# Kernel tuning notes

Hardware: AMD Instinct MI355X
Metric: run time of the kernel (lower is better)

Reference implementation:

```python
import jax, jax.numpy as jnp
import numpy as np

H = 14
N = H * H
DIM = 768
INT = 5
LAM = 3.5


def fft_conv_grouped(x, w):
    # x: (B, g*in_c, N) real; w: (g, int_c, in_c, H, H//2+1) complex
    g, int_c, in_c = w.shape[:3]
    B = x.shape[0]
    xf = jnp.fft.rfftn(x.reshape(B, g, in_c, H, H), axes=(-2, -1), norm='ortho')
    yf = jnp.einsum('bgchf,gichf->bgihf', xf, w)
    y = jnp.fft.irfftn(yf, s=(H, H), axes=(-2, -1), norm='ortho')
    return y.reshape(B, g * int_c, N)


def soft(x, t):
    # sign(x) * relu(|x| - t)
    return jnp.sign(x) * jnp.maximum(jnp.abs(x) - t, 0.0)


def batch_norm(x, gamma, beta, eps=1e-5):
    # training-mode BatchNorm1d applied per channel over (B, N); x: (B, N, C)
    m = x.mean(axis=(0, 1))
    v = x.var(axis=(0, 1))
    return (x - m) * jax.lax.rsqrt(v + eps) * gamma + beta


def setup_inputs() -> dict:
    key = jax.random.key(0)
    ks = jax.random.split(key, 8)
    B = 32
    Hf = H // 2 + 1
    # kernel: init randn*0.06, then normalize_parameters()
    kr = jax.random.normal(ks[0], (DIM, INT, 1, H, Hf, 2), dtype=jnp.float32) * 0.06
    kc = kr[..., 0] + 1j * kr[..., 1]
    nrm = jnp.sqrt((jnp.abs(kc) ** 2).sum(axis=(2, 3, 4), keepdims=True) * 2.0 / H ** 2)
    kc = kc / nrm
    kernel = jnp.stack([jnp.real(kc), jnp.imag(kc)], axis=-1)
    # L buffer: update_L(lam=1) -> per-group max singular value of Gram kk
    kk = jnp.einsum('gichf,gjchf->gijhf', kc, jnp.conj(kc))
    sv = np.linalg.svd(np.asarray(jnp.transpose(kk, (0, 3, 4, 1, 2))), compute_uv=False)
    L = jnp.asarray(sv.reshape(DIM, -1).max(axis=-1), dtype=jnp.float32)
    hid = 4 * DIM
    return {
        'x': jax.random.normal(ks[1], (B, N, DIM), dtype=jnp.float32),
        'v_w': jax.random.normal(ks[2], (DIM, DIM), dtype=jnp.float32) * 0.02,
        'proj_w': jax.random.normal(ks[3], (DIM, DIM), dtype=jnp.float32) * 0.02,
        'proj_b': jnp.zeros((DIM,), dtype=jnp.float32),
        'kernel': kernel,
        'kernel2': jax.random.normal(ks[4], (DIM, 1, 1, H, Hf, 2), dtype=jnp.float32) * 0.02,
        'n1_g': jnp.ones((DIM,), dtype=jnp.float32),
        'n1_b': jnp.zeros((DIM,), dtype=jnp.float32),
        'n2_g': jnp.ones((DIM,), dtype=jnp.float32),
        'n2_b': jnp.zeros((DIM,), dtype=jnp.float32),
        'fc1_w': jax.random.normal(ks[5], (hid, DIM), dtype=jnp.float32) * 0.02,
        'fc1_b': jnp.zeros((hid,), dtype=jnp.float32),
        'fc2_w': jax.random.normal(ks[6], (DIM, hid), dtype=jnp.float32) * 0.02,
        'fc2_b': jnp.zeros((DIM,), dtype=jnp.float32),
        'L': L,
    }


def reference(x, v_w, proj_w, proj_b, kernel, kernel2, n1_g, n1_b, n2_g, n2_b, fc1_w, fc1_b, fc2_w, fc2_b, L):
    k = kernel[..., 0] + 1j * kernel[..., 1]                 # (g, int, 1, H, Hf)
    kk = jnp.einsum('gichf,gjchf->gijhf', k, jnp.conj(k))     # (g, int, int, H, Hf)
    vx = x @ v_w.T                                            # v Linear, no bias
    xc = jnp.swapaxes(vx, -2, -1)                             # (B, C, N)
    u = fft_conv_grouped(xc, k)                               # (B, g*int, N)
    Lv = jnp.repeat(L, INT)[None, :, None]                    # (1, g*int, 1)
    # ISTA: init soft-threshold then 3 gradient + shrink steps
    s = soft(u, LAM)
    for _ in range(3):
        s = s - (fft_conv_grouped(s, kk) - u) / Lv
        s = soft(s, LAM / Lv)
    # reconstruct with conjugate-transposed kernel, then mix with kernel2
    new = fft_conv_grouped(s, jnp.swapaxes(jnp.conj(k), 1, 2))  # (B, g, N)
    k2 = kernel2[..., 0] + 1j * kernel2[..., 1]
    new = fft_conv_grouped(new, k2)
    new = jnp.swapaxes(new, -2, -1)                           # (B, N, C)
    new = x + (batch_norm(new, n1_g, n1_b) @ proj_w.T + proj_b)
    h = jax.nn.gelu(batch_norm(new, n2_g, n2_b) @ fc1_w.T + fc1_b, approximate=False)
    return new + (h @ fc2_w.T + fc2_b)
```

## Files before the change

kernel.cpp:

```cpp
#include <hip/hip_runtime.h>
#include <cmath>

typedef unsigned short u16;
typedef __bf16 bf16x8 __attribute__((ext_vector_type(8)));
typedef float f32x4 __attribute__((ext_vector_type(4)));
typedef float float4v __attribute__((ext_vector_type(4)));
typedef u16 ushort4v __attribute__((ext_vector_type(4)));
typedef u16 ushort8v __attribute__((ext_vector_type(8)));

#define DIMC 768
#define NP 196
#define MTOT 6272
#define HIDC 3072
#define LAMC 3.5f

__device__ const float C14d[14] = {
  1.0f, 0.9009688679024191f, 0.6234898018587336f, 0.22252093395631445f,
  -0.22252093395631445f, -0.6234898018587336f, -0.9009688679024191f, -1.0f,
  -0.9009688679024191f, -0.6234898018587336f, -0.22252093395631445f,
  0.22252093395631445f, 0.6234898018587336f, 0.9009688679024191f
};
__device__ const float S14d[14] = {
  0.0f, 0.43388373911755823f, 0.7818314824680298f, 0.9749279121818236f,
  0.9749279121818236f, 0.7818314824680298f, 0.43388373911755823f, 0.0f,
  -0.43388373911755823f, -0.7818314824680298f, -0.9749279121818236f,
  -0.9749279121818236f, -0.7818314824680298f, -0.43388373911755823f
};

__device__ __forceinline__ u16 f2bf(float f) {
  unsigned u = __builtin_bit_cast(unsigned, f);
  unsigned r = u + 0x7FFFu + ((u >> 16) & 1u);
  return (u16)(r >> 16);
}

__device__ __forceinline__ size_t fidx(int m, int k, int K) {
  return ((size_t)(m >> 4) * (K >> 5) + (k >> 5)) * 512 +
         (size_t)((((k >> 3) & 3) * 16 + (m & 15)) * 8 + (k & 7));
}

__global__ __launch_bounds__(256) void prep_k(
    const float* __restrict__ v_w, const float* __restrict__ fc2w,
    const float* __restrict__ x,
    u16* __restrict__ vwf, u16* __restrict__ fc2f, u16* __restrict__ xf,
    u16* __restrict__ Ff, u16* __restrict__ Gf) {
  const int bid = blockIdx.x, t = threadIdx.x;
  if (bid < 378) {
    int idx = bid * 256 + t;
    if (idx < 50176) {
      int j = idx & 7, lane = (idx >> 3) & 63;
      int mk = idx >> 9, k0 = mk % 7, m0 = mk / 7;
      int s = m0 * 16 + (lane & 15);
      int q = k0 * 32 + (lane >> 4) * 8 + j;
      float v = 0.f;
      if (q < 196) {
        int kr = s >> 4, f = (s >> 1) & 7, r = q / 14, c = q % 14;
        int th = (kr * r + f * c) % 14;
        v = (s & 1) ? -S14d[th] : C14d[th];
      }
      Ff[idx] = f2bf(v);
    } else {
      int t2 = idx - 50176;
      int j = t2 & 7, lane = (t2 >> 3) & 63;
      int pk = t2 >> 9, k0 = pk % 7, p0 = pk / 7;
      int p = p0 * 16 + (lane & 15);
      int s = k0 * 32 + (lane >> 4) * 8 + j;
      float v = 0.f;
      if (p < 196) {
        int kr = s >> 4, f = (s >> 1) & 7, r = p / 14, c = p % 14;
        int th = (kr * r + f * c) % 14;
        float w = (f == 0 || f == 7) ? 1.f : 2.f;
        v = (w * (1.f / 196.f)) * ((s & 1) ? -S14d[th] : C14d[th]);
      }
      Gf[t2] = f2bf(v);
    }
    return;
  }
  const float* src; u16* dst; int idx, K;
  if (bid < 666)        { src = v_w;  dst = vwf;  idx = (bid - 378) * 256 + t;  K = DIMC; }
  else if (bid < 1818)  { src = fc2w; dst = fc2f; idx = (bid - 666) * 256 + t;  K = HIDC; }
  else                  { src = x;    dst = xf;   idx = (bid - 1818) * 256 + t; K = DIMC; }
  const int KC = K >> 5;
  int chunk = idx >> 6, l = idx & 63;
  int row = (chunk / KC) * 16 + (l & 15);
  int k0 = (chunk % KC) * 32 + (l >> 4) * 8;
  const float* sp = src + (size_t)row * K + k0;
  float4v f0 = *(const float4v*)sp;
  float4v f1 = *(const float4v*)(sp + 4);
  ushort8v o;
#pragma unroll
  for (int j = 0; j < 4; ++j) { o[j] = f2bf(f0[j]); o[j + 4] = f2bf(f1[j]); }
  *(ushort8v*)(dst + (size_t)idx * 8) = o;
}

template<int EPI>
__global__ __launch_bounds__(256, 3) void gemmw_k(
    const u16* __restrict__ Af, const u16* __restrict__ Bf,
    const float* __restrict__ bias, const float* __restrict__ res,
    void* __restrict__ Cp, int Nr, int Kr, int NB) {
  const int t = threadIdx.x, w = t >> 6, lane = t & 63;
  const int bid = blockIdx.x;
  const int xcd = bid & 7, j = bid >> 3;
  const int mt = xcd + 8 * (j / NB);
  if (mt >= 98) return;
  const int m0 = mt * 64;
  const int n0 = ((j % NB) * 4 + w) * 64;
  const int KC = Kr >> 5;
  const int l15 = lane & 15, l4 = lane >> 4;

  const u16* Ab = Af + ((size_t)(m0 >> 4) * KC) * 512 + lane * 8;
  const u16* Bb = Bf + ((size_t)(n0 >> 4) * KC) * 512 + lane * 8;

  f32x4 acc[4][4];
#pragma unroll
  for (int a = 0; a < 4; ++a)
#pragma unroll
    for (int b2 = 0; b2 < 4; ++b2) acc[a][b2] = (f32x4){0.f, 0.f, 0.f, 0.f};

  bf16x8 a0[4], b0[4], a1[4], b1[4];
#pragma unroll
  for (int mb = 0; mb < 4; ++mb) a0[mb] = *(const bf16x8*)(Ab + ((size_t)mb * KC) * 512);
#pragma unroll
  for (int nb = 0; nb < 4; ++nb) b0[nb] = *(const bf16x8*)(Bb + ((size_t)nb * KC) * 512);

  for (int kc = 0; kc < KC; kc += 2) {
#pragma unroll
    for (int mb = 0; mb < 4; ++mb)
      a1[mb] = *(const bf16x8*)(Ab + ((size_t)mb * KC + kc + 1) * 512);
#pragma unroll
    for (int nb = 0; nb < 4; ++nb)
      b1[nb] = *(const bf16x8*)(Bb + ((size_t)nb * KC + kc + 1) * 512);
    __builtin_amdgcn_s_setprio(1);
#pragma unroll
    for (int mb = 0; mb < 4; ++mb)
#pragma unroll
      for (int nb = 0; nb < 4; ++nb)
        acc[mb][nb] = __builtin_amdgcn_mfma_f32_16x16x32_bf16(a0[mb], b0[nb], acc[mb][nb], 0, 0, 0);
    __builtin_amdgcn_s_setprio(0);
    if (kc + 2 < KC) {
#pragma unroll
      for (int mb = 0; mb < 4; ++mb)
        a0[mb] = *(const bf16x8*)(Ab + ((size_t)mb * KC + kc + 2) * 512);
#pragma unroll
      for (int nb = 0; nb < 4; ++nb)
        b0[nb] = *(const bf16x8*)(Bb + ((size_t)nb * KC + kc + 2) * 512);
    }
    __builtin_amdgcn_s_setprio(1);
#pragma unroll
    for (int mb = 0; mb < 4; ++mb)
#pragma unroll
      for (int nb = 0; nb < 4; ++nb)
        acc[mb][nb] = __builtin_amdgcn_mfma_f32_16x16x32_bf16(a1[mb], b1[nb], acc[mb][nb], 0, 0, 0);
    __builtin_amdgcn_s_setprio(0);
  }

#pragma unroll
  for (int mb = 0; mb < 4; ++mb) {
#pragma unroll
    for (int nb = 0; nb < 4; ++nb) {
      int n = n0 + nb * 16 + l15;
      if (EPI == 0) {
        int m0r = m0 + mb * 16 + l4 * 4;
        int bb = m0r / 196, np0 = m0r - bb * 196;
        *(float4v*)&((float*)Cp)[((size_t)bb * DIMC + n) * 196 + np0] =
            (float4v){acc[mb][nb][0], acc[mb][nb][1], acc[mb][nb][2], acc[mb][nb][3]};
      } else {
#pragma unroll
        for (int r = 0; r < 4; ++r) {
          int m = m0 + mb * 16 + l4 * 4 + r;
          float v = acc[mb][nb][r];
          if (EPI == 1) {
            ((float*)Cp)[(size_t)m * Nr + n] = v + bias[n] + res[(size_t)m * Nr + n];
          } else {
            float vb = v + bias[n];
            float ge = 0.5f * vb * (1.f + erff(vb * 0.70710678118654752f));
            ((u16*)Cp)[fidx(m, n, Nr)] = f2bf(ge);
          }
        }
      }
    }
  }
}

__global__ __launch_bounds__(64) void xf_k(
    const float* __restrict__ vxt, const u16* __restrict__ Ff,
    float* __restrict__ xfg) {
  const int lane = threadIdx.x;
  const int wgb = blockIdx.x;
  const int g = wgb >> 1, bhalf = wgb & 1;
  const int tl = lane & 15, h = lane >> 4;
  const float* xbase = vxt + ((size_t)(bhalf * 16 + tl) * DIMC + g) * 196;

  bf16x8 Bx[7];
#pragma unroll
  for (int k0 = 0; k0 < 7; ++k0) {
    int q0 = k0 * 32 + h * 8;
    ushort8v tv;
    if (k0 < 6) {
      float4v f0 = *(const float4v*)(xbase + q0);
      float4v f1 = *(const float4v*)(xbase + q0 + 4);
#pragma unroll
      for (int j = 0; j < 4; ++j) { tv[j] = f2bf(f0[j]); tv[j + 4] = f2bf(f1[j]); }
    } else {
#pragma unroll
      for (int j = 0; j < 8; ++j) {
        int q = q0 + j;
        tv[j] = (q < 196) ? f2bf(xbase[q]) : (u16)0;
      }
    }
    Bx[k0] = __builtin_bit_cast(bf16x8, tv);
  }

  float* xo = xfg + (size_t)wgb * (16 * 224);
  for (int m0 = 0; m0 < 14; ++m0) {
    f32x4 acc = (f32x4){0.f, 0.f, 0.f, 0.f};
#pragma unroll
    for (int k0 = 0; k0 < 7; ++k0) {
      bf16x8 Af = __builtin_bit_cast(bf16x8,
          *(const ushort8v*)(Ff + ((size_t)(m0 * 7 + k0) * 64 + lane) * 8));
      acc = __builtin_amdgcn_mfma_f32_16x16x32_bf16(Af, Bx[k0], acc, 0, 0, 0);
    }
    *(f32x4*)&xo[tl * 224 + m0 * 16 + h * 4] = acc;
  }
}

__global__ __launch_bounds__(64) void screen_k(
    const float* __restrict__ xfg, const float* __restrict__ kern,
    const u16* __restrict__ Gf, int* __restrict__ cnt, int* __restrict__ wl) {
  const int lane = threadIdx.x;
  const int bid = blockIdx.x;
  const int gb = bid / 5, i = bid - gb * 5;
  const int g = gb >> 1, bhalf = gb & 1;
  const int tl = lane & 15, h = lane >> 4;
  const float* xo = xfg + (size_t)gb * (16 * 224);
  const float* kb = kern + ((size_t)g * 5 + i) * 224;

  bf16x8 By[7];
#pragma unroll
  for (int k0 = 0; k0 < 7; ++k0) {
    f32x4 x0 = *(const f32x4*)&xo[tl * 224 + k0 * 32 + h * 8];
    f32x4 x1 = *(const f32x4*)&xo[tl * 224 + k0 * 32 + h * 8 + 4];
    int mb = k0 * 16 + h * 4;
    float2 ka = *(const float2*)(kb + (mb + 0) * 2);
    float2 kc = *(const float2*)(kb + (mb + 1) * 2);
    float2 ke = *(const float2*)(kb + (mb + 2) * 2);
    float2 kg = *(const float2*)(kb + (mb + 3) * 2);
    ushort8v tv;
    tv[0] = f2bf(ka.x * x0[0] - ka.y * x0[1]);
    tv[1] = f2bf(ka.x * x0[1] + ka.y * x0[0]);
    tv[2] = f2bf(kc.x * x0[2] - kc.y * x0[3]);
    tv[3] = f2bf(kc.x * x0[3] + kc.y * x0[2]);
    tv[4] = f2bf(ke.x * x1[0] - ke.y * x1[1]);
    tv[5] = f2bf(ke.x * x1[1] + ke.y * x1[0]);
    tv[6] = f2bf(kg.x * x1[2] - kg.y * x1[3]);
    tv[7] = f2bf(kg.x * x1[3] + kg.y * x1[2]);
    By[k0] = __builtin_bit_cast(bf16x8, tv);
  }

  float vmax = 0.f;
  for (int pp = 0; pp < 6; ++pp) {
    int p0 = pp * 2;
    f32x4 a0 = (f32x4){0.f, 0.f, 0.f, 0.f};
    f32x4 a1 = a0;
#pragma unroll
    for (int k0 = 0; k0 < 7; ++k0) {
      bf16x8 Ag0 = __builtin_bit_cast(bf16x8,
          *(const ushort8v*)(Gf + ((size_t)(p0 * 7 + k0) * 64 + lane) * 8));
      bf16x8 Ag1 = __builtin_bit_cast(bf16x8,
          *(const ushort8v*)(Gf + ((size_t)((p0 + 1) * 7 + k0) * 64 + lane) * 8));
      a0 = __builtin_amdgcn_mfma_f32_16x16x32_bf16(Ag0, By[k0], a0, 0, 0, 0);
      a1 = __builtin_amdgcn_mfma_f32_16x16x32_bf16(Ag1, By[k0], a1, 0, 0, 0);
    }
#pragma unroll
    for (int r = 0; r < 4; ++r) {
      vmax = fmaxf(vmax, fabsf(a0[r]));
      vmax = fmaxf(vmax, fabsf(a1[r]));
    }
  }
  {
    f32x4 a0 = (f32x4){0.f, 0.f, 0.f, 0.f};
#pragma unroll
    for (int k0 = 0; k0 < 7; ++k0) {
      bf16x8 Ag = __builtin_bit_cast(bf16x8,
          *(const ushort8v*)(Gf + ((size_t)(12 * 7 + k0) * 64 + lane) * 8));
      a0 = __builtin_amdgcn_mfma_f32_16x16x32_bf16(Ag, By[k0], a0, 0, 0, 0);
    }
#pragma unroll
    for (int r = 0; r < 4; ++r) vmax = fmaxf(vmax, fabsf(a0[r]));
  }

  vmax = fmaxf(vmax, __shfl_xor(vmax, 16));
  vmax = fmaxf(vmax, __shfl_xor(vmax, 32));
  if (lane < 16 && vmax > (LAMC - 0.1f)) {
    int idx = atomicAdd(cnt, 1);
    wl[idx] = g * 32 + bhalf * 16 + lane;
  }
}

__global__ __launch_bounds__(64) void slow_k(
    const float* __restrict__ vxt, const float* __restrict__ kern,
    const float* __restrict__ kern2, const float* __restrict__ Lbuf,
    const int* __restrict__ cnt, const int* __restrict__ wl,
    float* __restrict__ outp,
    float* __restrict__ tsum, float* __restrict__ tsq,
    unsigned* __restrict__ maskg, unsigned* __restrict__ bmask) {
  const int ntile = *cnt;
  if ((int)blockIdx.x >= ntile) return;
  const int t = threadIdx.x;
  __shared__ float TC[196], TSn[196];
  __shared__ float xs[196];
  __shared__ float t1R[112], t1I[112];
  __shared__ float t2R[112], t2I[112];
  __shared__ float zr[112], zi[112];
  __shared__ float kR[5][112], kI[5][112];
  __shared__ float uu[5][196];
  __shared__ float ss[5][196];
  __shared__ float k2R[112], k2I[112];

  for (int i = t; i < 196; i += 64) {
    int a = i / 14, c = i - (i / 14) * 14;
    int m = (a * c) % 14;
    TC[i] = C14d[m]; TSn[i] = S14d[m];
  }

  auto rowsFwd = [&](const float* xsrc) {
    for (int i = t; i < 112; i += 64) {
      int r = i >> 3, f = i & 7;
      const float* xp = xsrc + r * 14;
      const float* tc = &TC[f * 14]; const float* tsn = &TSn[f * 14];
      float ar = 0.f, ai = 0.f;
#pragma unroll
      for (int c = 0; c < 14; ++c) { float xv = xp[c]; ar += xv * tc[c]; ai -= xv * tsn[c]; }
      t1R[i] = ar; t1I[i] = ai;
    }
    __syncthreads();
  };
  auto colsFwd = [&](float* oR, float* oI) {
    for (int i = t; i < 112; i += 64) {
      int kr = i >> 3, f = i & 7;
      const float* tc = &TC[kr * 14]; const float* tsn = &TSn[kr * 14];
      float br = 0.f, bi = 0.f;
#pragma unroll
      for (int r = 0; r < 14; ++r) {
        float xr = t1R[r * 8 + f], xi = t1I[r * 8 + f];
        br += tc[r] * xr + tsn[r] * xi;
        bi += tc[r] * xi - tsn[r] * xr;
      }
      oR[i] = br; oI[i] = bi;
    }
    __syncthreads();
  };
  auto colsInv = [&]() {
    for (int i = t; i < 112; i += 64) {
      int r = i >> 3, f = i & 7;
      const float* tc = &TC[r * 14]; const float* tsn = &TSn[r * 14];
      float br = 0.f, bi = 0.f;
#pragma unroll
      for (int kr = 0; kr < 14; ++kr) {
        float xr = t1R[kr * 8 + f], xi = t1I[kr * 8 + f];
        br += tc[kr] * xr - tsn[kr] * xi;
        bi += tc[kr] * xi + tsn[kr] * xr;
      }
      t2R[i] = br; t2I[i] = bi;
    }
    __syncthreads();
  };
  auto rowVal = [&](int r, int c) -> float {
    const float* pR = &t2R[r * 8]; const float* pI = &t2I[r * 8];
    float v = pR[0] + ((c & 1) ? -pR[7] : pR[7]);
    float s2 = 0.f;
#pragma unroll
    for (int f = 1; f < 7; ++f) s2 += pR[f] * TC[f * 14 + c] - pI[f] * TSn[f * 14 + c];
    return (v + 2.f * s2) * (1.0f / 196.0f);
  };

  for (int widx = blockIdx.x; widx < ntile; widx += gridDim.x) {
    const int tile = wl[widx];
    const int g = tile >> 5, b = tile & 31;
    __syncthreads();
    for (int i = t; i < 560; i += 64) {
      int ii = i / 112, p = i - ii * 112;
      const float* kp = kern + ((size_t)g * 5 + ii) * 224 + p * 2;
      kR[ii][p] = kp[0]; kI[ii][p] = kp[1];
    }
    for (int i = t; i < 196; i += 64) xs[i] = vxt[((size_t)b * DIMC + g) * 196 + i];
    for (int i = t; i < 112; i += 64) {
      k2R[i] = kern2[(size_t)g * 224 + i * 2];
      k2I[i] = kern2[(size_t)g * 224 + i * 2 + 1];
    }
    __syncthreads();

    rowsFwd(xs);
    colsFwd(zr, zi);
    for (int ii = 0; ii < 5; ++ii) {
      for (int i = t; i < 112; i += 64) {
        float a = kR[ii][i], b2 = kI[ii][i];
        t1R[i] = a * zr[i] - b2 * zi[i];
        t1I[i] = a * zi[i] + b2 * zr[i];
      }
      __syncthreads();
      colsInv();
      for (int i = t; i < 196; i += 64) uu[ii][i] = rowVal(i / 14, i - (i / 14) * 14);
      __syncthreads();
    }

    const float invL = 1.0f / Lbuf[g];
    const float thr = LAMC * invL;
    {
      float* up = &uu[0][0];
      float* sp = &ss[0][0];
      for (int i = t; i < 980; i += 64) {
        float v = up[i];
        float a = fabsf(v) - LAMC;
        sp[i] = a > 0.f ? copysignf(a, v) : 0.f;
      }
    }
    __syncthreads();

    for (int iter = 0; iter < 4; ++iter) {
      for (int i = t; i < 112; i += 64) { zr[i] = 0.f; zi[i] = 0.f; }
      __syncthreads();
      for (int ii = 0; ii < 5; ++ii) {
        rowsFwd(&ss[ii][0]);
        colsFwd(t2R, t2I);
        for (int i = t; i < 112; i += 64) {
          float a = kR[ii][i], b2 = kI[ii][i];
          zr[i] += a * t2R[i] + b2 * t2I[i];
          zi[i] += a * t2I[i] - b2 * t2R[i];
        }
        __syncthreads();
      }
      if (iter == 3) break;
      for (int ii = 0; ii < 5; ++ii) {
        for (int i = t; i < 112; i += 64) {
          float a = kR[ii][i], b2 = kI[ii][i];
          t1R[i] = a * zr[i] - b2 * zi[i];
          t1I[i] = a * zi[i] + b2 * zr[i];
        }
        __syncthreads();
        colsInv();
        for (int i = t; i < 196; i += 64) {
          float v = rowVal(i / 14, i - (i / 14) * 14);
          float sv = ss[ii][i] - (v - uu[ii][i]) * invL;
          float aa = fabsf(sv) - thr;
          ss[ii][i] = aa > 0.f ? copysignf(aa, sv) : 0.f;
        }
        __syncthreads();
      }
    }

    if (t < 28) {
      int kr = t >> 1, f = (t & 1) * 7;
      int d = kr * 8 + f;
      int srci = ((14 - kr) % 14) * 8 + f;
      float pr = 0.5f * (zr[d] + zr[srci]);
      float pi = 0.5f * (zi[d] - zi[srci]);
      zr[d] = pr; zi[d] = pi;
    }
    __syncthreads();
    for (int i = t; i < 112; i += 64) {
      float a = k2R[i], b2 = k2I[i];
      t1R[i] = a * zr[i] - b2 * zi[i];
      t1I[i] = a * zi[i] + b2 * zr[i];
    }
    __syncthreads();
    colsInv();
    float sacc = 0.f, qacc = 0.f;
    for (int i = t; i < 196; i += 64) {
      float v = rowVal(i / 14, i - (i / 14) * 14);
      outp[((size_t)(b * 196 + i)) * DIMC + g] = v;
      sacc += v; qacc += v * v;
    }
#pragma unroll
    for (int off = 32; off; off >>= 1) {
      sacc += __shfl_xor(sacc, off);
      qacc += __shfl_xor(qacc, off);
    }
    if (t == 0) {
      tsum[tile] = sacc; tsq[tile] = qacc;
      atomicOr(&maskg[g], 1u << b);
      atomicOr(bmask, 1u << b);
    }
  }
}

__global__ __launch_bounds__(256) void stats1c0_k(
    const float* __restrict__ tsum, const float* __restrict__ tsq,
    const unsigned* __restrict__ maskg,
    const float* __restrict__ gam, const float* __restrict__ bet,
    const float* __restrict__ projw, const float* __restrict__ pb,
    float* __restrict__ sc1, float* __restrict__ c0) {
  __shared__ float sh1s[768];
  const int t = threadIdx.x;
  for (int c = t; c < DIMC; c += 256) {
    unsigned mask = maskg[c];
    float S = 0.f, Q = 0.f;
    if (mask) {
      for (int b = 0; b < 32; ++b)
        if ((mask >> b) & 1) { S += tsum[c * 32 + b]; Q += tsq[c * 32 + b]; }
    }
    float m = S * (1.0f / 6272.0f);
    float v = fmaxf(Q * (1.0f / 6272.0f) - m * m, 0.f);
    float rs = rsqrtf(v + 1e-5f);
    float sc = gam[c] * rs;
    sh1s[c] = bet[c] - m * sc;
    if (blockIdx.x == 0) sc1[c] = sc;
  }
  __syncthreads();
  int n = blockIdx.x * 256 + t;
  const float* row = projw + (size_t)n * DIMC;
  float s = 0.f;
  for (int g = 0; g < DIMC; g += 4) {
    float4v r = *(const float4v*)(row + g);
    s += r[0] * sh1s[g] + r[1] * sh1s[g + 1] + r[2] * sh1s[g + 2] + r[3] * sh1s[g + 3];
  }
  c0[n] = s + pb[n];
}

__global__ __launch_bounds__(256) void bnb_k(
    const float* __restrict__ x, const float* __restrict__ c0,
    const float* __restrict__ sc1, const unsigned* __restrict__ maskg,
    const unsigned* __restrict__ bmask, const float* __restrict__ newm,
    const float* __restrict__ projw,
    float* __restrict__ new2, u16* __restrict__ n2f,
    float* __restrict__ part) {
  const int jb = blockIdx.x, b = blockIdx.y, t = threadIdx.x;
  __shared__ unsigned gm[24];
  __shared__ float c0s[768];
  const bool hasb = ((*bmask >> b) & 1u) != 0u;
  if (t < 24) {
    unsigned w = 0;
    if (hasb)
      for (int j2 = 0; j2 < 32; ++j2) w |= ((maskg[t * 32 + j2] >> b) & 1u) << j2;
    gm[t] = w;
  }
  for (int c = t; c < 768; c += 256) c0s[c] = c0[c];
  __syncthreads();

  float S0 = 0, S1 = 0, S2 = 0, Q0 = 0, Q1 = 0, Q2 = 0;
  for (int mr = 0; mr < 7; ++mr) {
    int m = b * 196 + jb * 7 + mr;
    size_t row = (size_t)m * DIMC;
#pragma unroll
    for (int j2 = 0; j2 < 3; ++j2) {
      int n = t + j2 * 256;
      float v = x[row + n] + c0s[n];
      if (hasb) {
        for (int w = 0; w < 24; ++w) {
          unsigned bits = gm[w];
          while (bits) {
            int g = w * 32 + __builtin_ctz(bits);
            bits &= bits - 1;
            v += sc1[g] * newm[row + g] * projw[(size_t)n * DIMC + g];
          }
        }
      }
      new2[row + n] = v;
      n2f[fidx(m, n, DIMC)] = f2bf(v);
      if (j2 == 0) { S0 += v; Q0 += v * v; }
      else if (j2 == 1) { S1 += v; Q1 += v * v; }
      else { S2 += v; Q2 += v * v; }
    }
  }
  float* p = part + (size_t)(b * 28 + jb) * 1536;
  p[t] = S0; p[t + 256] = S1; p[t + 512] = S2;
  p[768 + t] = Q0; p[768 + 256 + t] = Q1; p[768 + 512 + t] = Q2;
}

__global__ __launch_bounds__(256) void red2_k(const float* __restrict__ part,
                                              float* __restrict__ part2) {
  int slot = blockIdx.x * 256 + threadIdx.x;
  int b = blockIdx.y;
  float s = 0.f;
  const float* p = part + (size_t)(b * 28) * 1536 + slot;
  for (int jb = 0; jb < 28; ++jb) s += p[(size_t)jb * 1536];
  part2[(size_t)b * 1536 + slot] = s;
}

__global__ __launch_bounds__(256) void stats2fin_k(const float* __restrict__ part2,
    const float* __restrict__ gam, const float* __restrict__ bet,
    float* __restrict__ scale, float* __restrict__ shift) {
  int c = blockIdx.x * 256 + threadIdx.x;
  float S = 0.f, Q = 0.f;
  for (int b = 0; b < 32; ++b) {
    S += part2[(size_t)b * 1536 + c];
    Q += part2[(size_t)b * 1536 + 768 + c];
  }
  float m = S * (1.0f / 6272.0f);
  float v = fmaxf(Q * (1.0f / 6272.0f) - m * m, 0.f);
  float rs = rsqrtf(v + 1e-5f);
  float sc = gam[c] * rs;
  scale[c] = sc;
  shift[c] = bet[c] - m * sc;
}

__global__ __launch_bounds__(256) void foldfc1_k(const float* __restrict__ fc1w,
    const float* __restrict__ fc1b, const float* __restrict__ sc2,
    const float* __restrict__ sh2, u16* __restrict__ fc1s,
    float* __restrict__ d0) {
  const int bid = blockIdx.x, t = threadIdx.x;
  if (bid < 12) {
    int n = bid * 256 + t;
    const float* row = fc1w + (size_t)n * DIMC;
    float s = 0.f;
    for (int k = 0; k < DIMC; k += 4) {
      float4v r = *(const float4v*)(row + k);
      float4v h = *(const float4v*)(sh2 + k);
      s += r[0] * h[0] + r[1] * h[1] + r[2] * h[2] + r[3] * h[3];
    }
    d0[n] = s + fc1b[n];
  } else {
    int idx = (bid - 12) * 256 + t;
    int chunk = idx >> 6, l = idx & 63;
    int n = (chunk / 24) * 16 + (l & 15);
    int k0 = (chunk % 24) * 32 + (l >> 4) * 8;
    const float* sp = fc1w + (size_t)n * DIMC + k0;
    float4v f0 = *(const float4v*)sp;
    float4v f1 = *(const float4v*)(sp + 4);
    float4v s0 = *(const float4v*)(sc2 + k0);
    float4v s1 = *(const float4v*)(sc2 + k0 + 4);
    f0 = f0 * s0; f1 = f1 * s1;
    ushort8v o;
#pragma unroll
    for (int j = 0; j < 4; ++j) { o[j] = f2bf(f0[j]); o[j + 4] = f2bf(f1[j]); }
    *(ushort8v*)(fc1s + (size_t)idx * 8) = o;
  }
}

extern "C" void kernel_launch(void* const* d_in, const int* in_sizes, int n_in,
                              void* d_out, int out_size, void* d_ws, size_t ws_size,
                              hipStream_t stream) {
  (void)in_sizes; (void)n_in; (void)out_size;
  const float* x      = (const float*)d_in[0];
  const float* v_w    = (const float*)d_in[1];
  const float* proj_w = (const float*)d_in[2];
  const float* proj_b = (const float*)d_in[3];
  const float* kern   = (const float*)d_in[4];
  const float* kern2  = (const float*)d_in[5];
  const float* n1g    = (const float*)d_in[6];
  const float* n1b    = (const float*)d_in[7];
  const float* n2g    = (const float*)d_in[8];
  const float* n2b    = (const float*)d_in[9];
  const float* fc1w   = (const float*)d_in[10];
  const float* fc1b   = (const float*)d_in[11];
  const float* fc2w   = (const float*)d_in[12];
  const float* fc2b   = (const float*)d_in[13];
  const float* Lb     = (const float*)d_in[14];
  float* out = (float*)d_out;

  char* ws = (char*)d_ws;
  size_t o = 0;
  auto alloc = [&](size_t bytes) { size_t r = o; o += (bytes + 255) & ~(size_t)255; return r; };
  u16*   vwf    = (u16*)(ws + alloc(589824 * 2));
  u16*   fc2f   = (u16*)(ws + alloc(2359296 * 2));
  u16*   fc1s   = (u16*)(ws + alloc(2359296 * 2));
  u16*   Ffb    = (u16*)(ws + alloc(50176 * 2));
  u16*   Gfb    = (u16*)(ws + alloc(46592 * 2));
  float* sc1    = (float*)(ws + alloc(768 * 4));
  float* sc2    = (float*)(ws + alloc(768 * 4));
  float* sh2    = (float*)(ws + alloc(768 * 4));
  float* c0     = (float*)(ws + alloc(768 * 4));
  float* d0     = (float*)(ws + alloc(3072 * 4));
  float* part   = (float*)(ws + alloc((size_t)896 * 1536 * 4));
  float* part2  = (float*)(ws + alloc((size_t)32 * 1536 * 4));
  char*  zblk   = (char*)(ws + alloc(4096));
  int*      cnt   = (int*)zblk;
  unsigned* bmask = (unsigned*)(zblk + 4);
  unsigned* maskg = (unsigned*)(zblk + 8);
  int*   wl     = (int*)(ws + alloc(131072 * 4));
  float* tsum   = (float*)(ws + alloc(24576 * 4));
  float* tsq    = (float*)(ws + alloc(24576 * 4));
  float* xfg    = (float*)(ws + alloc((size_t)1536 * 16 * 224 * 4));
  u16*   xf     = (u16*)(ws + alloc((size_t)MTOT * DIMC * 2));
  u16*   n2f    = (u16*)(ws + alloc((size_t)MTOT * DIMC * 2));
  float* vxt    = (float*)(ws + alloc((size_t)MTOT * DIMC * 4));
  float* newm   = (float*)(ws + alloc((size_t)MTOT * DIMC * 4));
  float* new2   = (float*)(ws + alloc((size_t)MTOT * DIMC * 4));
  u16*   hbf    = (u16*)vxt;
  if (ws_size < o) return;

  hipMemsetAsync(zblk, 0, 4096, stream);

  prep_k<<<4170, 256, 0, stream>>>(v_w, fc2w, x, vwf, fc2f, xf, Ffb, Gfb);
  gemmw_k<0><<<312, 256, 0, stream>>>(xf, vwf, nullptr, nullptr, vxt, DIMC, DIMC, 3);
  xf_k<<<1536, 64, 0, stream>>>(vxt, Ffb, xfg);
  screen_k<<<7680, 64, 0, stream>>>(xfg, kern, Gfb, cnt, wl);
  slow_k<<<1024, 64, 0, stream>>>(vxt, kern, kern2, Lb, cnt, wl, newm,
                                  tsum, tsq, maskg, bmask);
  stats1c0_k<<<3, 256, 0, stream>>>(tsum, tsq, maskg, n1g, n1b, proj_w, proj_b, sc1, c0);
  bnb_k<<<dim3(28, 32), 256, 0, stream>>>(x, c0, sc1, maskg, bmask, newm, proj_w,
                                          new2, n2f, part);
  red2_k<<<dim3(6, 32), 256, 0, stream>>>(part, part2);
  stats2fin_k<<<3, 256, 0, stream>>>(part2, n2g, n2b, sc2, sh2);
  foldfc1_k<<<1164, 256, 0, stream>>>(fc1w, fc1b, sc2, sh2, fc1s, d0);
  gemmw_k<2><<<1248, 256, 0, stream>>>(n2f, fc1s, d0, nullptr, hbf, HIDC, DIMC, 12);
  gemmw_k<1><<<312, 256, 0, stream>>>(hbf, fc2f, fc2b, new2, out, DIMC, HIDC, 3);
}
```

Baseline: 284.3 us.

## Dedupe screened tiles via bitmask flags and simplify GEMM main loop

The screen kernel no longer appends one worklist entry per (tile, i) hit. It ORs per-tile bits into a per-group flag word, and a new compact kernel turns the flags into a deduplicated worklist. This removes duplicate tiles across the 5 intermediate channels, along with the atomic contention and redundant slow_k work they cause. Separately, the GEMM drops its register double-buffering, setprio and the occupancy hint for a simple single-stage loop, which may expose load latency. The extra launch adds a small fixed cost.

```diff
diff --git a/kernel.cpp b/kernel.cpp
--- a/kernel.cpp
+++ b/kernel.cpp
@@ -93,7 +93,7 @@
 }
 
 template<int EPI>
-__global__ __launch_bounds__(256, 3) void gemmw_k(
+__global__ __launch_bounds__(256) void gemmw_k(
     const u16* __restrict__ Af, const u16* __restrict__ Bf,
     const float* __restrict__ bias, const float* __restrict__ res,
     void* __restrict__ Cp, int Nr, int Kr, int NB) {
@@ -116,41 +116,19 @@
 #pragma unroll
     for (int b2 = 0; b2 < 4; ++b2) acc[a][b2] = (f32x4){0.f, 0.f, 0.f, 0.f};
 
-  bf16x8 a0[4], b0[4], a1[4], b1[4];
-#pragma unroll
-  for (int mb = 0; mb < 4; ++mb) a0[mb] = *(const bf16x8*)(Ab + ((size_t)mb * KC) * 512);
-#pragma unroll
-  for (int nb = 0; nb < 4; ++nb) b0[nb] = *(const bf16x8*)(Bb + ((size_t)nb * KC) * 512);
-
-  for (int kc = 0; kc < KC; kc += 2) {
+  for (int kc = 0; kc < KC; ++kc) {
+    bf16x8 af[4], bfv[4];
 #pragma unroll
     for (int mb = 0; mb < 4; ++mb)
-      a1[mb] = *(const bf16x8*)(Ab + ((size_t)mb * KC + kc + 1) * 512);
+      af[mb] = *(const bf16x8*)(Ab + ((size_t)mb * KC + kc) * 512);
 #pragma unroll
     for (int nb = 0; nb < 4; ++nb)
-      b1[nb] = *(const bf16x8*)(Bb + ((size_t)nb * KC + kc + 1) * 512);
-    __builtin_amdgcn_s_setprio(1);
+      bfv[nb] = *(const bf16x8*)(Bb + ((size_t)nb * KC + kc) * 512);
 #pragma unroll
     for (int mb = 0; mb < 4; ++mb)
 #pragma unroll
       for (int nb = 0; nb < 4; ++nb)
-        acc[mb][nb] = __builtin_amdgcn_mfma_f32_16x16x32_bf16(a0[mb], b0[nb], acc[mb][nb], 0, 0, 0);
-    __builtin_amdgcn_s_setprio(0);
-    if (kc + 2 < KC) {
-#pragma unroll
-      for (int mb = 0; mb < 4; ++mb)
-        a0[mb] = *(const bf16x8*)(Ab + ((size_t)mb * KC + kc + 2) * 512);
-#pragma unroll
-      for (int nb = 0; nb < 4; ++nb)
-        b0[nb] = *(const bf16x8*)(Bb + ((size_t)nb * KC + kc + 2) * 512);
-    }
-    __builtin_amdgcn_s_setprio(1);
-#pragma unroll
-    for (int mb = 0; mb < 4; ++mb)
-#pragma unroll
-      for (int nb = 0; nb < 4; ++nb)
-        acc[mb][nb] = __builtin_amdgcn_mfma_f32_16x16x32_bf16(a1[mb], b1[nb], acc[mb][nb], 0, 0, 0);
-    __builtin_amdgcn_s_setprio(0);
+        acc[mb][nb] = __builtin_amdgcn_mfma_f32_16x16x32_bf16(af[mb], bfv[nb], acc[mb][nb], 0, 0, 0);
   }
 
 #pragma unroll
@@ -225,7 +203,7 @@
 
 __global__ __launch_bounds__(64) void screen_k(
     const float* __restrict__ xfg, const float* __restrict__ kern,
-    const u16* __restrict__ Gf, int* __restrict__ cnt, int* __restrict__ wl) {
+    const u16* __restrict__ Gf, unsigned* __restrict__ tflag) {
   const int lane = threadIdx.x;
   const int bid = blockIdx.x;
   const int gb = bid / 5, i = bid - gb * 5;
@@ -233,12 +211,13 @@
   const int tl = lane & 15, h = lane >> 4;
   const float* xo = xfg + (size_t)gb * (16 * 224);
   const float* kb = kern + ((size_t)g * 5 + i) * 224;
+  (void)tl;
 
   bf16x8 By[7];
 #pragma unroll
   for (int k0 = 0; k0 < 7; ++k0) {
-    f32x4 x0 = *(const f32x4*)&xo[tl * 224 + k0 * 32 + h * 8];
-    f32x4 x1 = *(const f32x4*)&xo[tl * 224 + k0 * 32 + h * 8 + 4];
+    f32x4 x0 = *(const f32x4*)&xo[(lane & 15) * 224 + k0 * 32 + h * 8];
+    f32x4 x1 = *(const f32x4*)&xo[(lane & 15) * 224 + k0 * 32 + h * 8 + 4];
     int mb = k0 * 16 + h * 4;
     float2 ka = *(const float2*)(kb + (mb + 0) * 2);
     float2 kc = *(const float2*)(kb + (mb + 1) * 2);
@@ -290,9 +269,23 @@
 
   vmax = fmaxf(vmax, __shfl_xor(vmax, 16));
   vmax = fmaxf(vmax, __shfl_xor(vmax, 32));
-  if (lane < 16 && vmax > (LAMC - 0.1f)) {
+  unsigned long long ball = __ballot(vmax > (LAMC - 0.1f));
+  unsigned bits = (unsigned)(ball & 0xFFFFull);
+  if (lane == 0 && bits)
+    atomicOr(&tflag[g], bits << (bhalf * 16));
+}
+
+__global__ __launch_bounds__(256) void compact_k(const unsigned* __restrict__ tflag,
+                                                 int* __restrict__ cnt,
+                                                 int* __restrict__ wl) {
+  int wd = blockIdx.x * 256 + threadIdx.x;
+  if (wd >= 768) return;
+  unsigned bits = tflag[wd];
+  while (bits) {
+    int b = __builtin_ctz(bits);
+    bits &= bits - 1;
     int idx = atomicAdd(cnt, 1);
-    wl[idx] = g * 32 + bhalf * 16 + lane;
+    wl[idx] = wd * 32 + b;
   }
 }
 
@@ -662,11 +655,12 @@
   float* d0     = (float*)(ws + alloc(3072 * 4));
   float* part   = (float*)(ws + alloc((size_t)896 * 1536 * 4));
   float* part2  = (float*)(ws + alloc((size_t)32 * 1536 * 4));
-  char*  zblk   = (char*)(ws + alloc(4096));
+  char*  zblk   = (char*)(ws + alloc(8192));
   int*      cnt   = (int*)zblk;
   unsigned* bmask = (unsigned*)(zblk + 4);
   unsigned* maskg = (unsigned*)(zblk + 8);
-  int*   wl     = (int*)(ws + alloc(131072 * 4));
+  unsigned* tflag = (unsigned*)(zblk + 4096);
+  int*   wl     = (int*)(ws + alloc(24576 * 4));
   float* tsum   = (float*)(ws + alloc(24576 * 4));
   float* tsq    = (float*)(ws + alloc(24576 * 4));
   float* xfg    = (float*)(ws + alloc((size_t)1536 * 16 * 224 * 4));
@@ -678,12 +672,13 @@
   u16*   hbf    = (u16*)vxt;
   if (ws_size < o) return;
 
-  hipMemsetAsync(zblk, 0, 4096, stream);
+  hipMemsetAsync(zblk, 0, 8192, stream);
 
   prep_k<<<4170, 256, 0, stream>>>(v_w, fc2w, x, vwf, fc2f, xf, Ffb, Gfb);
   gemmw_k<0><<<312, 256, 0, stream>>>(xf, vwf, nullptr, nullptr, vxt, DIMC, DIMC, 3);
   xf_k<<<1536, 64, 0, stream>>>(vxt, Ffb, xfg);
-  screen_k<<<7680, 64, 0, stream>>>(xfg, kern, Gfb, cnt, wl);
+  screen_k<<<7680, 64, 0, stream>>>(xfg, kern, Gfb, tflag);
+  compact_k<<<3, 256, 0, stream>>>(tflag, cnt, wl);
   slow_k<<<1024, 64, 0, stream>>>(vxt, kern, kern2, Lb, cnt, wl, newm,
                                   tsum, tsq, maskg, bmask);
   stats1c0_k<<<3, 256, 0, stream>>>(tsum, tsq, maskg, n1g, n1b, proj_w, proj_b, sc1, c0);
```

Result: no change. 285.9 us (+0.5%).
